# Kernel optimization log

Measured on AMD Instinct MI355X. Metric: run time of the kernel, lower is better.

Reference implementation:

```python
import jax, jax.numpy as jnp
import numpy as np

N_NODES = 50000
N_EDGES = 800000
F_IN = 128
OUT_DIM = 121
NEG_SLOPE = 0.2  # LeakyReLU slope in GAT attention


def gat_layer(x, src, dst, W, a_src, a_dst, W_res, merge, act, n_nodes):
    """One multi-head GAT layer with residual connection.
    x: [N, F_in]; W: [F_in, H*U]; a_src/a_dst: [H, U]; W_res: [F_in, D_out] or None.
    """
    H, U = a_src.shape
    h = (x @ W).reshape(n_nodes, H, U)                       # [N,H,U]
    e_s = jnp.einsum('nhu,hu->nh', h, a_src)                 # [N,H]
    e_d = jnp.einsum('nhu,hu->nh', h, a_dst)                 # [N,H]
    e = jax.nn.leaky_relu(e_s[src] + e_d[dst], NEG_SLOPE)    # [E,H] per-edge logits
    # segment softmax over incoming edges of each destination node
    m = jax.ops.segment_max(e, dst, num_segments=n_nodes)    # [N,H]
    m = jnp.where(jnp.isfinite(m), m, 0.0)                   # nodes with no in-edges
    p = jnp.exp(e - m[dst])                                  # [E,H]
    denom = jax.ops.segment_sum(p, dst, num_segments=n_nodes)
    alpha = p / jnp.maximum(denom[dst], 1e-9)                # [E,H]
    msg = alpha[:, :, None] * h[src]                         # [E,H,U]
    out = jax.ops.segment_sum(msg, dst, num_segments=n_nodes)  # [N,H,U]
    if merge == 'concat':
        out = out.reshape(n_nodes, H * U)
    else:  # 'avg'
        out = out.mean(axis=1)
    res = x if W_res is None else x @ W_res
    return act(out + res)


def setup_inputs() -> dict:
    key = jax.random.key(0)
    ks = jax.random.split(key, 13)
    s = 0.05
    x = jax.random.normal(ks[0], (N_NODES, F_IN), jnp.float32)
    edges = jax.random.randint(ks[1], (N_EDGES, 2), 0, N_NODES, jnp.int32)
    return {
        'input_features': x,
        'edges': edges,
        # layer 1: 128 units, 4 heads, concat -> 512
        'W1': s * jax.random.normal(ks[2], (F_IN, 4 * 128), jnp.float32),
        'a1_src': s * jax.random.normal(ks[3], (4, 128), jnp.float32),
        'a1_dst': s * jax.random.normal(ks[4], (4, 128), jnp.float32),
        'R1': s * jax.random.normal(ks[5], (F_IN, 4 * 128), jnp.float32),
        # layer 2: 128 units, 4 heads, concat -> 512 (residual is identity: dims match)
        'W2': s * jax.random.normal(ks[6], (512, 4 * 128), jnp.float32),
        'a2_src': s * jax.random.normal(ks[7], (4, 128), jnp.float32),
        'a2_dst': s * jax.random.normal(ks[8], (4, 128), jnp.float32),
        # layer 3: 121 units, 6 heads, avg -> 121
        'W3': s * jax.random.normal(ks[9], (512, 6 * OUT_DIM), jnp.float32),
        'a3_src': s * jax.random.normal(ks[10], (6, OUT_DIM), jnp.float32),
        'a3_dst': s * jax.random.normal(ks[11], (6, OUT_DIM), jnp.float32),
        'R3': s * jax.random.normal(ks[12], (512, OUT_DIM), jnp.float32),
    }


def reference(input_features, edges, W1, a1_src, a1_dst, R1,
              W2, a2_src, a2_dst, W3, a3_src, a3_dst, R3):
    src, dst = edges[:, 0], edges[:, 1]
    elu = jax.nn.elu
    ident = lambda z: z
    x = gat_layer(input_features, src, dst, W1, a1_src, a1_dst, R1,
                  'concat', elu, N_NODES)
    x = gat_layer(x, src, dst, W2, a2_src, a2_dst, None,
                  'concat', elu, N_NODES)
    out = gat_layer(x, src, dst, W3, a3_src, a3_dst, R3,
                    'avg', ident, N_NODES)
    return out
```

## Files before the change

kernel.cpp:

```cpp
#include <hip/hip_runtime.h>
#include <math.h>

#define NN 50000
#define NE 800000
#define MBLK 391
#define ROWQ 48
#define ROWR 7

typedef __attribute__((ext_vector_type(8))) short  short8;
typedef __attribute__((ext_vector_type(4))) short  short4v;
typedef __attribute__((ext_vector_type(4))) float  floatx4;
typedef signed char schar8 __attribute__((ext_vector_type(8)));

__device__ __forceinline__ float bf2f(unsigned short u) {
    union { unsigned int i; float f; } v; v.i = ((unsigned int)u) << 16; return v.f;
}
__device__ __forceinline__ unsigned short f2bf(float f) {
    union { float f; unsigned int i; } v; v.f = f;
    unsigned int i = v.i;
    i += 0x7FFFu + ((i >> 16) & 1u);
    return (unsigned short)(i >> 16);
}

__device__ __forceinline__ float leaky(float v) { return (v > 0.f) ? v : 0.2f * v; }

__device__ __forceinline__ void gload_lds16(const unsigned short* g, unsigned short* l) {
    __builtin_amdgcn_global_load_lds(
        (const __attribute__((address_space(1))) unsigned int*)g,
        (__attribute__((address_space(3))) unsigned int*)l, 16, 0, 0);
}

__global__ void deg_kernel(const int* __restrict__ edges, int* __restrict__ deg, int E) {
    int e = blockIdx.x * blockDim.x + threadIdx.x;
    if (e < E) atomicAdd(&deg[edges[2 * e + 1]], 1);
}

__global__ void scan_kernel(const int* __restrict__ deg, int* __restrict__ row_ptr,
                            int* __restrict__ cursor, int n) {
    __shared__ int sums[256];
    int t = threadIdx.x;
    const int C = (n + 255) / 256;
    int lo = t * C, hi = min(lo + C, n);
    if (lo > n) lo = n;
    if (hi < lo) hi = lo;
    int s = 0;
    for (int i = lo; i < hi; ++i) s += deg[i];
    sums[t] = s;
    __syncthreads();
    for (int off = 1; off < 256; off <<= 1) {
        int v = (t >= off) ? sums[t - off] : 0;
        __syncthreads();
        sums[t] += v;
        __syncthreads();
    }
    int run = (t == 0) ? 0 : sums[t - 1];
    for (int i = lo; i < hi; ++i) {
        int d = deg[i];
        row_ptr[i] = run;
        cursor[i]  = run;
        run += d;
    }
    if (t == 255) row_ptr[n] = sums[255];
}

__global__ void scatter_kernel(const int* __restrict__ edges, int* __restrict__ cursor,
                               int* __restrict__ edge_src, int* __restrict__ edge_dst, int E) {
    int e = blockIdx.x * blockDim.x + threadIdx.x;
    if (e < E) {
        int sv = edges[2 * e], d = edges[2 * e + 1];
        int pos = atomicAdd(&cursor[d], 1);
        if (pos >= 0 && pos < E) { edge_src[pos] = sv; edge_dst[pos] = d; }
    }
}

template <int H>
__global__ __launch_bounds__(256) void pw_kernel(const float* __restrict__ e_s,
                                                 const float* __restrict__ e_d,
                                                 const int* __restrict__ esrc,
                                                 const int* __restrict__ edst,
                                                 float* __restrict__ pw, int E) {
    int e = blockIdx.x * blockDim.x + threadIdx.x;
    if (e >= E) return;
    int s = esrc[e], d = edst[e];
    const float* ps = e_s + (size_t)s * H;
    const float* pd = e_d + (size_t)d * H;
#pragma unroll
    for (int h = 0; h < H; ++h)
        pw[(size_t)e * H + h] = __expf(leaky(ps[h] + pd[h]));
}

__global__ __launch_bounds__(256) void prep2(
    const float* __restrict__ W1, const float* __restrict__ R1,
    const float* __restrict__ W2, const float* __restrict__ W3,
    const float* __restrict__ R3, const float* __restrict__ a1s,
    const float* __restrict__ a1d, const float* __restrict__ a3s,
    const float* __restrict__ a3d, const float* __restrict__ x0,
    unsigned short* __restrict__ w1t, unsigned short* __restrict__ r1t,
    unsigned short* __restrict__ w2t, unsigned short* __restrict__ w3t,
    unsigned short* __restrict__ r3t, float* __restrict__ wsb,
    float* __restrict__ wdb, float* __restrict__ a3sp, float* __restrict__ a3dp,
    int* __restrict__ deg, unsigned short* __restrict__ x0b) {
    const int b = blockIdx.x, t = threadIdx.x;

    if (b >= 3532) {
        int i = ((b - 3532) * 256 + t) * 4;
        if (i + 3 < NN * 128) {
            float4 v = *(const float4*)(x0 + i);
            ushort4 o;
            o.x = f2bf(v.x); o.y = f2bf(v.y); o.z = f2bf(v.z); o.w = f2bf(v.w);
            *(ushort4*)(x0b + i) = o;
        }
        return;
    }
    if (b >= 3336) {
        int i = (b - 3336) * 256 + t;
        if (i < NN) deg[i] = 0;
        return;
    }

    int idx = b * 256 + t;
    if (idx < 65536) {
        int n = idx >> 7, k = idx & 127;
        w1t[idx] = f2bf(W1[k * 512 + n]);
        return;
    }
    idx -= 65536;
    if (idx < 65536) {
        int n = idx >> 7, k = idx & 127;
        r1t[idx] = f2bf(R1[k * 512 + n]);
        return;
    }
    idx -= 65536;
    if (idx < 262144) {
        int n = idx >> 9, k = idx & 511;
        w2t[idx] = f2bf(W2[(size_t)k * 512 + n]);
        return;
    }
    idx -= 262144;
    if (idx < 393216) {
        int np = idx >> 9, k = idx & 511;
        int h = np >> 7, u = np & 127;
        w3t[idx] = f2bf((u < 121) ? W3[(size_t)k * 726 + h * 121 + u] : 0.f);
        return;
    }
    idx -= 393216;
    if (idx < 65536) {
        int n = idx >> 9, k = idx & 511;
        r3t[idx] = f2bf((n < 121) ? R3[(size_t)k * 121 + n] : 0.f);
        return;
    }
    idx -= 65536;
    if (idx < 512) {
        int h = idx >> 7, k = idx & 127;
        float s = 0.f, d = 0.f;
        for (int u = 0; u < 128; ++u) {
            float w = W1[k * 512 + h * 128 + u];
            s = fmaf(w, a1s[h * 128 + u], s);
            d = fmaf(w, a1d[h * 128 + u], d);
        }
        wsb[idx] = s;
        wdb[idx] = d;
        return;
    }
    idx -= 512;
    if (idx < 1536) {
        int which = (idx >= 768) ? 1 : 0;
        int j = idx - which * 768;
        int h = j >> 7, u = j & 127;
        float val = (u < 121) ? (which ? a3d[h * 121 + u] : a3s[h * 121 + u]) : 0.f;
        if (which) a3dp[j] = val; else a3sp[j] = val;
    }
}

__global__ __launch_bounds__(256) void gemm_esc(const unsigned short* __restrict__ A,
                                                const unsigned short* __restrict__ BT,
                                                signed char* __restrict__ Cq,
                                                float2* __restrict__ esq,
                                                float* __restrict__ e_d,
                                                const float* __restrict__ asv,
                                                const float* __restrict__ adv,
                                                float* __restrict__ resout,
                                                int M, int NS, int Hl, int NX) {
    __shared__ __align__(16) unsigned short As[128 * 32];
    __shared__ __align__(16) unsigned short Bs[128 * 32];

    const int xcd = blockIdx.x & 7, pos = blockIdx.x >> 3;
    const int nrows = ROWQ + (xcd < ROWR ? 1 : 0);
    if (pos >= nrows * NX) return;
    const int ybase = xcd * ROWQ + min(xcd, ROWR);
    const int by = ybase + pos / NX;
    const int bx = pos - (pos / NX) * NX;

    const int t    = threadIdx.x;
    const int wave = t >> 6, lane = t & 63;
    const int wm   = (wave >> 1) * 64, wn = (wave & 1) * 64;
    const int l15  = lane & 15, q = lane >> 4;
    const int row0 = by * 128, col0 = bx * 128;

    floatx4 acc[4][4];
#pragma unroll
    for (int i = 0; i < 4; ++i)
#pragma unroll
        for (int j = 0; j < 4; ++j) acc[i][j] = (floatx4){0.f, 0.f, 0.f, 0.f};

    for (int k0 = 0; k0 < 512; k0 += 32) {
#pragma unroll
        for (int p = 0; p < 2; ++p) {
            int idx = p * 256 + t;
            int r = idx >> 2, qq = idx & 3;
            int cc = qq ^ ((r >> 1) & 3);
            int ar = row0 + r; ar = (ar < M) ? ar : (M - 1);
            unsigned short* ldsA = As + (p * 2048 + wave * 512);
            unsigned short* ldsB = Bs + (p * 2048 + wave * 512);
            gload_lds16(A  + (size_t)ar * 512 + k0 + cc * 8, ldsA);
            gload_lds16(BT + (size_t)(col0 + r) * 512 + k0 + cc * 8, ldsB);
        }
        __syncthreads();

        short8 af[4], bfr[4];
#pragma unroll
        for (int mi = 0; mi < 4; ++mi) {
            int row = wm + 16 * mi + l15;
            af[mi] = *(const short8*)&As[row * 32 + (q ^ ((row >> 1) & 3)) * 8];
        }
#pragma unroll
        for (int ni = 0; ni < 4; ++ni) {
            int row = wn + 16 * ni + l15;
            bfr[ni] = *(const short8*)&Bs[row * 32 + (q ^ ((row >> 1) & 3)) * 8];
        }
#pragma unroll
        for (int mi = 0; mi < 4; ++mi)
#pragma unroll
            for (int ni = 0; ni < 4; ++ni)
                acc[mi][ni] = __builtin_amdgcn_mfma_f32_16x16x32_bf16(af[mi], bfr[ni], acc[mi][ni], 0, 0, 0);
        __syncthreads();
    }

    if (col0 == 768) {
#pragma unroll
        for (int ni = 0; ni < 4; ++ni) {
            int gcl = wn + 16 * ni + l15;
            if (gcl >= 121) continue;
#pragma unroll
            for (int mi = 0; mi < 4; ++mi) {
#pragma unroll
                for (int r = 0; r < 4; ++r) {
                    int gr = row0 + wm + 16 * mi + q * 4 + r;
                    if (gr < M) resout[(size_t)gr * 121 + gcl] = acc[mi][ni][r];
                }
            }
        }
        return;
    }

    float* sred  = (float*)As;
    int*   sredm = (int*)(sred + 256);
    if (t < 256) sred[t] = 0.f;
    if (t < 128) sredm[t] = 0;
    __syncthreads();

    float av[4], dv[4];
#pragma unroll
    for (int ni = 0; ni < 4; ++ni) {
        int gc = col0 + wn + 16 * ni + l15;
        av[ni] = asv[gc];
        dv[ni] = adv[gc];
    }
#pragma unroll
    for (int mi = 0; mi < 4; ++mi) {
#pragma unroll
        for (int r = 0; r < 4; ++r) {
            float ps = 0.f, pd = 0.f, mx = 0.f;
#pragma unroll
            for (int ni = 0; ni < 4; ++ni) {
                ps = fmaf(acc[mi][ni][r], av[ni], ps);
                pd = fmaf(acc[mi][ni][r], dv[ni], pd);
                mx = fmaxf(mx, fabsf(acc[mi][ni][r]));
            }
#pragma unroll
            for (int off = 1; off < 16; off <<= 1) {
                ps += __shfl_xor(ps, off);
                pd += __shfl_xor(pd, off);
                mx = fmaxf(mx, __shfl_xor(mx, off));
            }
            if (l15 == 0) {
                int rloc = wm + 16 * mi + 4 * q + r;
                atomicAdd(&sred[rloc * 2 + 0], ps);
                atomicAdd(&sred[rloc * 2 + 1], pd);
                atomicMax(&sredm[rloc], __float_as_int(mx));
            }
        }
    }
    __syncthreads();

#pragma unroll
    for (int mi = 0; mi < 4; ++mi) {
#pragma unroll
        for (int r = 0; r < 4; ++r) {
            int rloc = wm + 16 * mi + 4 * q + r;
            float rm = fmaxf(__int_as_float(sredm[rloc]), 1e-20f);
            float iq = 127.f / rm;
            int gr = row0 + rloc;
#pragma unroll
            for (int ni = 0; ni < 4; ++ni) {
                int gc = col0 + wn + 16 * ni + l15;
                if (gr < M)
                    Cq[(size_t)gr * NS + gc] = (signed char)(int)rintf(acc[mi][ni][r] * iq);
            }
        }
    }

    if (t < 128) {
        int gr = row0 + t;
        if (gr < M) {
            float2 ev;
            ev.x = sred[t * 2 + 0];
            ev.y = fmaxf(__int_as_float(sredm[t]), 1e-20f) * (1.f / 127.f);
            esq[(size_t)gr * Hl + bx] = ev;
            e_d[(size_t)gr * Hl + bx] = sred[t * 2 + 1];
        }
    }
}

__global__ __launch_bounds__(256) void gemm_l1(const unsigned short* __restrict__ aggx,
                                               const unsigned short* __restrict__ w1t,
                                               const unsigned short* __restrict__ x0b,
                                               const unsigned short* __restrict__ r1t,
                                               unsigned short* __restrict__ C, int M) {
    __shared__ __align__(16) unsigned short As[128 * 32];
    __shared__ __align__(16) unsigned short Bs[128 * 32];

    const int t    = threadIdx.x;
    const int wave = t >> 6, lane = t & 63;
    const int wm   = (wave >> 1) * 64, wn = (wave & 1) * 64;
    const int l15  = lane & 15, q = lane >> 4;
    const int row0 = blockIdx.y * 128;
    const int head = blockIdx.x;
    const int ccol = head * 128;

    floatx4 acc[4][4];
#pragma unroll
    for (int i = 0; i < 4; ++i)
#pragma unroll
        for (int j = 0; j < 4; ++j) acc[i][j] = (floatx4){0.f, 0.f, 0.f, 0.f};

    for (int ph = 0; ph < 2; ++ph) {
        const unsigned short* A  = ph ? x0b : (aggx + ccol);
        const int AS             = ph ? 128 : 512;
        const unsigned short* BT = (ph ? r1t : w1t) + (size_t)ccol * 128;

        for (int k0 = 0; k0 < 128; k0 += 32) {
#pragma unroll
            for (int p = 0; p < 2; ++p) {
                int idx = p * 256 + t;
                int r = idx >> 2, qq = idx & 3;
                int ar = row0 + r; ar = (ar < M) ? ar : (M - 1);
                unsigned short* ldsA = As + (p * 2048 + wave * 512);
                unsigned short* ldsB = Bs + (p * 2048 + wave * 512);
                gload_lds16(A  + (size_t)ar * AS + k0 + qq * 8, ldsA);
                gload_lds16(BT + (size_t)r * 128 + k0 + qq * 8, ldsB);
            }
            __syncthreads();

            short8 af[4], bfr[4];
#pragma unroll
            for (int mi = 0; mi < 4; ++mi) af[mi]  = *(const short8*)&As[(wm + 16 * mi + l15) * 32 + q * 8];
#pragma unroll
            for (int ni = 0; ni < 4; ++ni) bfr[ni] = *(const short8*)&Bs[(wn + 16 * ni + l15) * 32 + q * 8];
#pragma unroll
            for (int mi = 0; mi < 4; ++mi)
#pragma unroll
                for (int ni = 0; ni < 4; ++ni)
                    acc[mi][ni] = __builtin_amdgcn_mfma_f32_16x16x32_bf16(af[mi], bfr[ni], acc[mi][ni], 0, 0, 0);
            __syncthreads();
        }
    }

#pragma unroll
    for (int ni = 0; ni < 4; ++ni) {
        int gc = ccol + wn + 16 * ni + l15;
#pragma unroll
        for (int mi = 0; mi < 4; ++mi) {
#pragma unroll
            for (int r = 0; r < 4; ++r) {
                int gr = row0 + wm + 16 * mi + q * 4 + r;
                if (gr < M) {
                    float z = acc[mi][ni][r];
                    z = (z > 0.f) ? z : (__expf(z) - 1.f);
                    C[(size_t)gr * 512 + gc] = f2bf(z);
                }
            }
        }
    }
}

__global__ __launch_bounds__(256) void escore_x(const unsigned short* __restrict__ x,
                                                const float* __restrict__ ws,
                                                const float* __restrict__ wd,
                                                float* __restrict__ e_s,
                                                float* __restrict__ e_d) {
    const int wave = threadIdx.x >> 6, lane = threadIdx.x & 63;
    const int n = blockIdx.x * 4 + wave;
    const int h = lane >> 4, seg = lane & 15;

    short8 hv = *(const short8*)(x + (size_t)n * 128 + seg * 8);
    float4 w0 = *(const float4*)(ws + h * 128 + seg * 8);
    float4 w1 = *(const float4*)(ws + h * 128 + seg * 8 + 4);
    float4 d0 = *(const float4*)(wd + h * 128 + seg * 8);
    float4 d1 = *(const float4*)(wd + h * 128 + seg * 8 + 4);
    float av[8] = {w0.x, w0.y, w0.z, w0.w, w1.x, w1.y, w1.z, w1.w};
    float dv[8] = {d0.x, d0.y, d0.z, d0.w, d1.x, d1.y, d1.z, d1.w};

    float ps = 0.f, pd = 0.f;
#pragma unroll
    for (int j = 0; j < 8; ++j) {
        float xv = bf2f((unsigned short)hv[j]);
        ps = fmaf(xv, av[j], ps);
        pd = fmaf(xv, dv[j], pd);
    }
#pragma unroll
    for (int off = 1; off < 16; off <<= 1) {
        ps += __shfl_xor(ps, off);
        pd += __shfl_xor(pd, off);
    }
    if (seg == 0) {
        e_s[(size_t)n * 4 + h] = ps;
        e_d[(size_t)n * 4 + h] = pd;
    }
}

__global__ __launch_bounds__(256) void agg_x512(const unsigned short* __restrict__ x,
                                                const float* __restrict__ pw,
                                                const int* __restrict__ rowp,
                                                const int* __restrict__ esrc,
                                                unsigned short* __restrict__ aggx) {
    const int wave = threadIdx.x >> 6, lane = threadIdx.x & 63;
    const int n = blockIdx.x * 4 + wave;
    const int lid = lane & 31, half = lane >> 5;
    const int beg = rowp[n], end = rowp[n + 1];

    float den[4] = {0.f, 0.f, 0.f, 0.f};
    float acc[4][4];
#pragma unroll
    for (int h = 0; h < 4; ++h)
#pragma unroll
        for (int j = 0; j < 4; ++j) acc[h][j] = 0.f;

    int e = beg;
    for (; e + 8 <= end; e += 8) {
        int s[4];
        float4 p[4];
        short4v xr[4];
#pragma unroll
        for (int k = 0; k < 4; ++k) s[k] = esrc[e + 2 * k + half];
#pragma unroll
        for (int k = 0; k < 4; ++k) p[k] = *(const float4*)(pw + (size_t)(e + 2 * k + half) * 4);
#pragma unroll
        for (int k = 0; k < 4; ++k) xr[k] = *(const short4v*)(x + (size_t)s[k] * 128 + lid * 4);
#pragma unroll
        for (int k = 0; k < 4; ++k) {
            den[0] += p[k].x; den[1] += p[k].y; den[2] += p[k].z; den[3] += p[k].w;
#pragma unroll
            for (int j = 0; j < 4; ++j) {
                float xf = bf2f((unsigned short)xr[k][j]);
                acc[0][j] = fmaf(p[k].x, xf, acc[0][j]);
                acc[1][j] = fmaf(p[k].y, xf, acc[1][j]);
                acc[2][j] = fmaf(p[k].z, xf, acc[2][j]);
                acc[3][j] = fmaf(p[k].w, xf, acc[3][j]);
            }
        }
    }
    for (; e < end; e += 2) {
        int idx = e + half;
        if (idx < end) {
            int s = esrc[idx];
            float4 p = *(const float4*)(pw + (size_t)idx * 4);
            short4v xr = *(const short4v*)(x + (size_t)s * 128 + lid * 4);
            den[0] += p.x; den[1] += p.y; den[2] += p.z; den[3] += p.w;
#pragma unroll
            for (int j = 0; j < 4; ++j) {
                float xf = bf2f((unsigned short)xr[j]);
                acc[0][j] = fmaf(p.x, xf, acc[0][j]);
                acc[1][j] = fmaf(p.y, xf, acc[1][j]);
                acc[2][j] = fmaf(p.z, xf, acc[2][j]);
                acc[3][j] = fmaf(p.w, xf, acc[3][j]);
            }
        }
    }

#pragma unroll
    for (int h = 0; h < 4; ++h) {
        den[h] += __shfl_xor(den[h], 32);
#pragma unroll
        for (int j = 0; j < 4; ++j) acc[h][j] += __shfl_xor(acc[h][j], 32);
    }
    if (half == 0) {
#pragma unroll
        for (int h = 0; h < 4; ++h) {
            const float inv = 1.f / fmaxf(den[h], 1e-9f);
            ushort4 o;
            o.x = f2bf(acc[h][0] * inv);
            o.y = f2bf(acc[h][1] * inv);
            o.z = f2bf(acc[h][2] * inv);
            o.w = f2bf(acc[h][3] * inv);
            *(ushort4*)(aggx + (size_t)n * 512 + h * 128 + lid * 4) = o;
        }
    }
}

__global__ __launch_bounds__(256) void agg_q512(const signed char* __restrict__ hq,
                                                const float2* __restrict__ esq,
                                                const float* __restrict__ ed,
                                                const int* __restrict__ rowp,
                                                const int* __restrict__ esrc,
                                                const unsigned short* res,
                                                unsigned short* out) {
    const int wave = threadIdx.x >> 6, lane = threadIdx.x & 63;
    const int n = blockIdx.x * 4 + wave;
    const int h = lane >> 4;
    const int beg = rowp[n], end = rowp[n + 1];
    const float edh = ed[(size_t)n * 4 + h];

    float den = 0.f;
    float acc[8];
#pragma unroll
    for (int j = 0; j < 8; ++j) acc[j] = 0.f;

    int e = beg;
    for (; e + 8 <= end; e += 8) {
        int s[8];
#pragma unroll
        for (int k = 0; k < 8; ++k) s[k] = esrc[e + k];
        schar8 r[8];
#pragma unroll
        for (int k = 0; k < 8; ++k) r[k] = *(const schar8*)(hq + (size_t)s[k] * 512 + lane * 8);
        float p[8], qv[8];
#pragma unroll
        for (int k = 0; k < 8; ++k) {
            float2 ev = esq[(size_t)s[k] * 4 + h];
            float pv = __expf(leaky(ev.x + edh));
            p[k] = pv;
            qv[k] = pv * ev.y;
        }
#pragma unroll
        for (int k = 0; k < 8; ++k) den += p[k];
#pragma unroll
        for (int j = 0; j < 8; ++j) {
            float a = acc[j];
#pragma unroll
            for (int k = 0; k < 8; ++k) a = fmaf(qv[k], (float)r[k][j], a);
            acc[j] = a;
        }
    }
    for (; e < end; ++e) {
        int s0 = esrc[e];
        schar8 r0 = *(const schar8*)(hq + (size_t)s0 * 512 + lane * 8);
        float2 ev = esq[(size_t)s0 * 4 + h];
        float p0 = __expf(leaky(ev.x + edh));
        float q0 = p0 * ev.y;
        den += p0;
#pragma unroll
        for (int j = 0; j < 8; ++j) acc[j] = fmaf(q0, (float)r0[j], acc[j]);
    }

    const float inv = 1.f / fmaxf(den, 1e-9f);
    short8 rv = *(const short8*)(res + (size_t)n * 512 + lane * 8);
    short8 ov;
#pragma unroll
    for (int j = 0; j < 8; ++j) {
        float z = acc[j] * inv + bf2f((unsigned short)rv[j]);
        z = (z > 0.f) ? z : (__expf(z) - 1.f);
        ov[j] = (short)f2bf(z);
    }
    *(short8*)(out + (size_t)n * 512 + lane * 8) = ov;
}

__global__ __launch_bounds__(256) void agg_q768(const signed char* __restrict__ hq,
                                                const float2* __restrict__ esq,
                                                const float* __restrict__ ed,
                                                const int* __restrict__ rowp,
                                                const int* __restrict__ esrc,
                                                const float* res,
                                                float* out) {
    __shared__ float s_vals[4][768];
    const int wave = threadIdx.x >> 6, lane = threadIdx.x & 63;
    const int n = blockIdx.x * 4 + wave;
    const int beg = rowp[n], end = rowp[n + 1];

    const int h0 = lane >> 4;
    const bool has1 = (lane < 32);
    const int h1 = 4 + (lane >> 4);
    const float edh0 = ed[(size_t)n * 6 + h0];
    const float edh1 = has1 ? ed[(size_t)n * 6 + h1] : 0.f;

    float den0 = 0.f, den1 = 0.f;
    float acc0[8], acc1[8];
#pragma unroll
    for (int j = 0; j < 8; ++j) { acc0[j] = 0.f; acc1[j] = 0.f; }

    int e = beg;
    for (; e + 4 <= end; e += 4) {
        int s[4];
#pragma unroll
        for (int k = 0; k < 4; ++k) s[k] = esrc[e + k];
        schar8 r0[4];
#pragma unroll
        for (int k = 0; k < 4; ++k) r0[k] = *(const schar8*)(hq + (size_t)s[k] * 768 + lane * 8);
        float p0[4], q0[4];
#pragma unroll
        for (int k = 0; k < 4; ++k) {
            float2 ev = esq[(size_t)s[k] * 6 + h0];
            float pv = __expf(leaky(ev.x + edh0));
            p0[k] = pv;
            q0[k] = pv * ev.y;
        }
        den0 += (p0[0] + p0[1]) + (p0[2] + p0[3]);
#pragma unroll
        for (int j = 0; j < 8; ++j)
            acc0[j] = fmaf(q0[0], (float)r0[0][j],
                      fmaf(q0[1], (float)r0[1][j],
                      fmaf(q0[2], (float)r0[2][j],
                      fmaf(q0[3], (float)r0[3][j], acc0[j]))));
        if (has1) {
            schar8 r1[4];
#pragma unroll
            for (int k = 0; k < 4; ++k) r1[k] = *(const schar8*)(hq + (size_t)s[k] * 768 + 512 + lane * 8);
            float p1[4], q1[4];
#pragma unroll
            for (int k = 0; k < 4; ++k) {
                float2 ev = esq[(size_t)s[k] * 6 + h1];
                float pv = __expf(leaky(ev.x + edh1));
                p1[k] = pv;
                q1[k] = pv * ev.y;
            }
            den1 += (p1[0] + p1[1]) + (p1[2] + p1[3]);
#pragma unroll
            for (int j = 0; j < 8; ++j)
                acc1[j] = fmaf(q1[0], (float)r1[0][j],
                          fmaf(q1[1], (float)r1[1][j],
                          fmaf(q1[2], (float)r1[2][j],
                          fmaf(q1[3], (float)r1[3][j], acc1[j]))));
        }
    }
    for (; e < end; ++e) {
        int s = esrc[e];
        schar8 r0 = *(const schar8*)(hq + (size_t)s * 768 + lane * 8);
        float2 ev0 = esq[(size_t)s * 6 + h0];
        float p0 = __expf(leaky(ev0.x + edh0));
        float q0 = p0 * ev0.y;
        den0 += p0;
#pragma unroll
        for (int j = 0; j < 8; ++j) acc0[j] = fmaf(q0, (float)r0[j], acc0[j]);
        if (has1) {
            schar8 r1 = *(const schar8*)(hq + (size_t)s * 768 + 512 + lane * 8);
            float2 ev1 = esq[(size_t)s * 6 + h1];
            float p1 = __expf(leaky(ev1.x + edh1));
            float q1 = p1 * ev1.y;
            den1 += p1;
#pragma unroll
            for (int j = 0; j < 8; ++j) acc1[j] = fmaf(q1, (float)r1[j], acc1[j]);
        }
    }

    const float inv0 = 1.f / fmaxf(den0, 1e-9f);
#pragma unroll
    for (int j = 0; j < 8; ++j) s_vals[wave][lane * 8 + j] = acc0[j] * inv0;
    if (has1) {
        const float inv1 = 1.f / fmaxf(den1, 1e-9f);
#pragma unroll
        for (int j = 0; j < 8; ++j) s_vals[wave][512 + lane * 8 + j] = acc1[j] * inv1;
    }
    __syncthreads();

    for (int u = lane; u < 121; u += 64) {
        float sum = 0.f;
#pragma unroll
        for (int hh = 0; hh < 6; ++hh) sum += s_vals[wave][hh * 128 + u];
        float v = sum * (1.f / 6.f) + res[(size_t)n * 121 + u];
        __builtin_nontemporal_store(v, out + (size_t)n * 121 + u);
    }
}

static inline size_t align256(size_t x) { return (x + 255) & ~(size_t)255; }

extern "C" void kernel_launch(void* const* d_in, const int* in_sizes, int n_in,
                              void* d_out, int out_size, void* d_ws, size_t ws_size,
                              hipStream_t stream) {
    const float* x0  = (const float*)d_in[0];
    const int* edges = (const int*)d_in[1];
    const float* W1  = (const float*)d_in[2];
    const float* a1s = (const float*)d_in[3];
    const float* a1d = (const float*)d_in[4];
    const float* R1  = (const float*)d_in[5];
    const float* W2  = (const float*)d_in[6];
    const float* a2s = (const float*)d_in[7];
    const float* a2d = (const float*)d_in[8];
    const float* W3  = (const float*)d_in[9];
    const float* a3s = (const float*)d_in[10];
    const float* a3d = (const float*)d_in[11];
    const float* R3  = (const float*)d_in[12];
    float* out = (float*)d_out;

    char* w = (char*)d_ws;
    size_t off = 0;
    unsigned short* hbuf = (unsigned short*)(w + off); off = align256(off + (size_t)NN * 768 * 2);
    unsigned short* x1   = (unsigned short*)(w + off); off = align256(off + (size_t)NN * 512 * 2);
    float* es  = (float*)(w + off); off = align256(off + (size_t)NN * 6 * 4);
    float* ed  = (float*)(w + off); off = align256(off + (size_t)NN * 6 * 4);
    int* rowp  = (int*)(w + off);   off = align256(off + (size_t)(NN + 1) * 4);
    int* esrc  = (int*)(w + off);   off = align256(off + (size_t)NE * 4);
    int* edst  = (int*)(w + off);   off = align256(off + (size_t)NE * 4);
    float* pw  = (float*)(w + off); off = align256(off + (size_t)NE * 4 * 4 + 256);
    unsigned short* w1t = (unsigned short*)(w + off); off = align256(off + (size_t)512 * 128 * 2);
    unsigned short* r1t = (unsigned short*)(w + off); off = align256(off + (size_t)512 * 128 * 2);
    unsigned short* w2t = (unsigned short*)(w + off); off = align256(off + (size_t)512 * 512 * 2);
    unsigned short* w3t = (unsigned short*)(w + off); off = align256(off + (size_t)768 * 512 * 2);
    unsigned short* r3t = (unsigned short*)(w + off); off = align256(off + (size_t)128 * 512 * 2);
    float* wsb = (float*)(w + off); off = align256(off + (size_t)512 * 4);
    float* wdb = (float*)(w + off); off = align256(off + (size_t)512 * 4);
    float* a3sp = (float*)(w + off); off = align256(off + (size_t)768 * 4);
    float* a3dp = (float*)(w + off); off = align256(off + (size_t)768 * 4);
    float2* esq = (float2*)(w + off); off = align256(off + (size_t)NN * 6 * 8);
    int* deg = (int*)es;
    int* cur = (int*)ed;
    unsigned short* x0b  = hbuf;
    unsigned short* aggx = hbuf + (size_t)NN * 128;
    signed char* hq = (signed char*)hbuf;
    (void)ws_size;

    const int EB = (NE + 255) / 256;
    const int MB = MBLK;
    const int AB = NN / 4;

    prep2<<<9782, 256, 0, stream>>>(W1, R1, W2, W3, R3, a1s, a1d, a3s, a3d, x0,
                                    w1t, r1t, w2t, w3t, r3t, wsb, wdb, a3sp, a3dp,
                                    deg, x0b);

    deg_kernel<<<EB, 256, 0, stream>>>(edges, deg, NE);
    scan_kernel<<<1, 256, 0, stream>>>(deg, rowp, cur, NN);
    scatter_kernel<<<EB, 256, 0, stream>>>(edges, cur, esrc, edst, NE);

    escore_x<<<AB, 256, 0, stream>>>(x0b, wsb, wdb, es, ed);
    pw_kernel<4><<<EB, 256, 0, stream>>>(es, ed, esrc, edst, pw, NE);
    agg_x512<<<AB, 256, 0, stream>>>(x0b, pw, rowp, esrc, aggx);
    gemm_l1<<<dim3(4, MB), 256, 0, stream>>>(aggx, w1t, x0b, r1t, x1, NN);

    gemm_esc<<<8 * 49 * 4, 256, 0, stream>>>(x1, w2t, hq, esq, ed,
                                             a2s, a2d, out, NN, 512, 4, 4);
    agg_q512<<<AB, 256, 0, stream>>>(hq, esq, ed, rowp, esrc, x1, x1);

    gemm_esc<<<8 * 49 * 7, 256, 0, stream>>>(x1, w3t, hq, esq, ed,
                                             a3sp, a3dp, out, NN, 768, 6, 7);
    agg_q768<<<AB, 256, 0, stream>>>(hq, esq, ed, rowp, esrc, out, out);
}
```

Baseline: 789.8 us.

## Process aggregation nodes in degree-sorted order to balance waves within blocks

The scan kernel now also builds a histogram of in-degrees (capped at 255) and an exclusive prefix over it. A new perm kernel counting-sorts node ids by degree, and the layer-2 and layer-3 aggregation kernels index nodes through this permutation. Each block's four waves then handle nodes of similar degree, which is meant to cut intra-block imbalance and tail waiting. The cost is an extra kernel with contended global atomics on a few degree bins, plus loss of the natural node-order locality for output and residual accesses.

```diff
diff --git a/kernel.cpp b/kernel.cpp
--- a/kernel.cpp
+++ b/kernel.cpp
@@ -36,15 +36,21 @@
 }
 
 __global__ void scan_kernel(const int* __restrict__ deg, int* __restrict__ row_ptr,
-                            int* __restrict__ cursor, int n) {
+                            int* __restrict__ cursor, int* __restrict__ binc, int n) {
     __shared__ int sums[256];
+    __shared__ int hist[256];
     int t = threadIdx.x;
+    hist[t] = 0;
     const int C = (n + 255) / 256;
     int lo = t * C, hi = min(lo + C, n);
     if (lo > n) lo = n;
     if (hi < lo) hi = lo;
     int s = 0;
-    for (int i = lo; i < hi; ++i) s += deg[i];
+    for (int i = lo; i < hi; ++i) {
+        int d = deg[i];
+        s += d;
+        atomicAdd(&hist[min(d, 255)], 1);
+    }
     sums[t] = s;
     __syncthreads();
     for (int off = 1; off < 256; off <<= 1) {
@@ -61,6 +67,14 @@
         run += d;
     }
     if (t == 255) row_ptr[n] = sums[255];
+    __syncthreads();
+    for (int off = 1; off < 256; off <<= 1) {
+        int v = (t >= off) ? hist[t - off] : 0;
+        __syncthreads();
+        hist[t] += v;
+        __syncthreads();
+    }
+    binc[t] = (t == 0) ? 0 : hist[t - 1];
 }
 
 __global__ void scatter_kernel(const int* __restrict__ edges, int* __restrict__ cursor,
@@ -70,6 +84,16 @@
         int sv = edges[2 * e], d = edges[2 * e + 1];
         int pos = atomicAdd(&cursor[d], 1);
         if (pos >= 0 && pos < E) { edge_src[pos] = sv; edge_dst[pos] = d; }
+    }
+}
+
+__global__ void perm_kernel(const int* __restrict__ deg, int* __restrict__ binc,
+                            int* __restrict__ perm, int n) {
+    int i = blockIdx.x * blockDim.x + threadIdx.x;
+    if (i < n) {
+        int b = min(deg[i], 255);
+        int pos = atomicAdd(&binc[b], 1);
+        perm[pos] = i;
     }
 }
 
@@ -513,10 +537,11 @@
                                                 const float* __restrict__ ed,
                                                 const int* __restrict__ rowp,
                                                 const int* __restrict__ esrc,
+                                                const int* __restrict__ perm,
                                                 const unsigned short* res,
                                                 unsigned short* out) {
     const int wave = threadIdx.x >> 6, lane = threadIdx.x & 63;
-    const int n = blockIdx.x * 4 + wave;
+    const int n = perm[blockIdx.x * 4 + wave];
     const int h = lane >> 4;
     const int beg = rowp[n], end = rowp[n + 1];
     const float edh = ed[(size_t)n * 4 + h];
@@ -580,11 +605,12 @@
                                                 const float* __restrict__ ed,
                                                 const int* __restrict__ rowp,
                                                 const int* __restrict__ esrc,
+                                                const int* __restrict__ perm,
                                                 const float* res,
                                                 float* out) {
     __shared__ float s_vals[4][768];
     const int wave = threadIdx.x >> 6, lane = threadIdx.x & 63;
-    const int n = blockIdx.x * 4 + wave;
+    const int n = perm[blockIdx.x * 4 + wave];
     const int beg = rowp[n], end = rowp[n + 1];
 
     const int h0 = lane >> 4;
@@ -721,6 +747,8 @@
     float* a3sp = (float*)(w + off); off = align256(off + (size_t)768 * 4);
     float* a3dp = (float*)(w + off); off = align256(off + (size_t)768 * 4);
     float2* esq = (float2*)(w + off); off = align256(off + (size_t)NN * 6 * 8);
+    int* perm = (int*)(w + off); off = align256(off + (size_t)NN * 4);
+    int* binc = (int*)(w + off); off = align256(off + (size_t)256 * 4);
     int* deg = (int*)es;
     int* cur = (int*)ed;
     unsigned short* x0b  = hbuf;
@@ -731,14 +759,16 @@
     const int EB = (NE + 255) / 256;
     const int MB = MBLK;
     const int AB = NN / 4;
+    const int NB = (NN + 255) / 256;
 
     prep2<<<9782, 256, 0, stream>>>(W1, R1, W2, W3, R3, a1s, a1d, a3s, a3d, x0,
                                     w1t, r1t, w2t, w3t, r3t, wsb, wdb, a3sp, a3dp,
                                     deg, x0b);
 
     deg_kernel<<<EB, 256, 0, stream>>>(edges, deg, NE);
-    scan_kernel<<<1, 256, 0, stream>>>(deg, rowp, cur, NN);
+    scan_kernel<<<1, 256, 0, stream>>>(deg, rowp, cur, binc, NN);
     scatter_kernel<<<EB, 256, 0, stream>>>(edges, cur, esrc, edst, NE);
+    perm_kernel<<<NB, 256, 0, stream>>>(deg, binc, perm, NN);
 
     escore_x<<<AB, 256, 0, stream>>>(x0b, wsb, wdb, es, ed);
     pw_kernel<4><<<EB, 256, 0, stream>>>(es, ed, esrc, edst, pw, NE);
@@ -747,9 +777,9 @@
 
     gemm_esc<<<8 * 49 * 4, 256, 0, stream>>>(x1, w2t, hq, esq, ed,
                                              a2s, a2d, out, NN, 512, 4, 4);
-    agg_q512<<<AB, 256, 0, stream>>>(hq, esq, ed, rowp, esrc, x1, x1);
+    agg_q512<<<AB, 256, 0, stream>>>(hq, esq, ed, rowp, esrc, perm, x1, x1);
 
     gemm_esc<<<8 * 49 * 7, 256, 0, stream>>>(x1, w3t, hq, esq, ed,
                                              a3sp, a3dp, out, NN, 768, 6, 7);
-    agg_q768<<<AB, 256, 0, stream>>>(hq, esq, ed, rowp, esrc, out, out);
-}
+    agg_q768<<<AB, 256, 0, stream>>>(hq, esq, ed, rowp, esrc, perm, out, out);
+}
```

New measurement: 936.0 us. 1.19x slower.
